# Kernel tuning notes

Hardware: AMD Instinct MI355X
Metric: run time of the kernel (lower is better)

## Reference

```python
import jax, jax.numpy as jnp
import numpy as np

D = 1024
H = 16
DH = D // H  # 64
EPS = 1e-6


def setup_inputs() -> dict:
    key = jax.random.key(0)
    ks = jax.random.split(key, 8)
    N, NQ, NK = 8, 1024, 1024
    queries = jax.random.normal(ks[0], (N, NQ, D), dtype=jnp.float32)
    keys = jax.random.normal(ks[1], (N, NK, D), dtype=jnp.float32)
    values = jax.random.normal(ks[2], (N, NK, D), dtype=jnp.float32)
    mask = jax.random.uniform(ks[3], (H * N, NQ, NK), dtype=jnp.float32)
    s = 1.0 / np.sqrt(D)
    Wq = jax.random.normal(ks[4], (H, DH, D), dtype=jnp.float32) * s  # per-head Linear(d, d_head) weights
    Wk = jax.random.normal(ks[5], (H, DH, D), dtype=jnp.float32) * s
    Wv = jax.random.normal(ks[6], (H, DH, D), dtype=jnp.float32) * s
    Wo = jax.random.normal(ks[7], (D, D), dtype=jnp.float32) * s
    return {"queries": queries, "keys": keys, "values": values, "mask": mask,
            "Wq": Wq, "Wk": Wk, "Wv": Wv, "Wo": Wo}


def reference(queries, keys, values, mask, Wq, Wk, Wv, Wo):
    N, NQ, _ = queries.shape
    NK = keys.shape[1]
    # per-head projections, fused into one batched einsum (head-major like torch.cat(dim=0))
    q = jnp.einsum('nqd,hed->hnqe', queries, Wq)  # [H, N, NQ, DH]
    k = jnp.einsum('nkd,hed->hnke', keys, Wk)
    v = jnp.einsum('nkd,hed->hnke', values, Wv)
    scores = jnp.einsum('hnqe,hnke->hnqk', q, k) / jnp.sqrt(jnp.float32(DH))
    att = jax.nn.softmax(scores, axis=-1)  # [H, N, NQ, NK]
    m = mask.reshape(H, N, NQ, NK)
    att = att * m
    att = att / (att.sum(axis=-1, keepdims=True) + EPS)
    o = jnp.einsum('hnqk,hnke->hnqe', att, v)  # [H, N, NQ, DH]
    # concat heads along feature dim: [N, NQ, H*DH]
    o = o.transpose(1, 2, 0, 3).reshape(N, NQ, D)
    return o @ Wo.T
```

## Files before the change

### kernel.cpp

```cpp
#include <hip/hip_runtime.h>
#include <stdint.h>

#define DEV static __device__ __forceinline__

typedef __attribute__((ext_vector_type(8))) short shortx8;
typedef __attribute__((ext_vector_type(4))) float floatx4;
typedef __attribute__((ext_vector_type(4))) unsigned short ushortx4;
typedef __attribute__((ext_vector_type(4))) unsigned int uintx4;


DEV unsigned short f2bf(float x) {
  unsigned int u = __float_as_uint(x);
  u += 0x7fffu + ((u >> 16) & 1u);
  return (unsigned short)(u >> 16);
}

DEV unsigned int cvtpk(float lo, float hi) {
  unsigned int r;
  asm("v_cvt_pk_bf16_f32 %0, %1, %2" : "=v"(r) : "v"(lo), "v"(hi));
  return r;
}

DEV void async16(const void* g, void* l) {
  __builtin_amdgcn_global_load_lds(
      (const __attribute__((address_space(1))) void*)g,
      (__attribute__((address_space(3))) void*)l, 16, 0, 0);
}

__global__ __launch_bounds__(256) void cast_all(
    const float* __restrict__ xq, const float* __restrict__ xk, const float* __restrict__ xv,
    const float* __restrict__ wq, const float* __restrict__ wk, const float* __restrict__ wv,
    const float* __restrict__ wo,
    unsigned short* __restrict__ oxq, unsigned short* __restrict__ oxk, unsigned short* __restrict__ oxv,
    unsigned short* __restrict__ owq, unsigned short* __restrict__ owk, unsigned short* __restrict__ owv,
    unsigned short* __restrict__ owo) {
  int b = blockIdx.x;
  const float* in;
  unsigned short* out;
  size_t i;
  if (b < 12288) {
    int which = b >> 12;
    in = which == 0 ? xq : (which == 1 ? xk : xv);
    out = which == 0 ? oxq : (which == 1 ? oxk : oxv);
    i = (size_t)(b & 4095) * 256 + threadIdx.x;
  } else {
    int bb = b - 12288;
    int which = bb >> 9;
    in = which == 0 ? wq : (which == 1 ? wk : (which == 2 ? wv : wo));
    out = which == 0 ? owq : (which == 1 ? owk : (which == 2 ? owv : owo));
    i = (size_t)(bb & 511) * 256 + threadIdx.x;
  }
  const floatx4* src = (const floatx4*)in;
  floatx4 a = src[2 * i];
  floatx4 c = src[2 * i + 1];
  uintx4 o;
  o[0] = cvtpk(a[0], a[1]);
  o[1] = cvtpk(a[2], a[3]);
  o[2] = cvtpk(c[0], c[1]);
  o[3] = cvtpk(c[2], c[3]);
  ((uintx4*)out)[i] = o;
}


__global__ __launch_bounds__(256) void gemm_qkv(
    const unsigned short* __restrict__ Xq, const unsigned short* __restrict__ Xk,
    const unsigned short* __restrict__ Xv,
    const unsigned short* __restrict__ Bq, const unsigned short* __restrict__ Bk,
    const unsigned short* __restrict__ Bv,
    unsigned short* __restrict__ Oq, unsigned short* __restrict__ Ok,
    unsigned short* __restrict__ Ov) {
  __shared__ __align__(16) unsigned short As[128 * 32];
  __shared__ __align__(16) unsigned short Bs[128 * 32];
  const int z = blockIdx.z;
  const unsigned short* A = z == 0 ? Xq : (z == 1 ? Xk : Xv);
  const unsigned short* B = z == 0 ? Bq : (z == 1 ? Bk : Bv);
  unsigned short* O = z == 0 ? Oq : (z == 1 ? Ok : Ov);

  const int tid  = threadIdx.x;
  const int lane = tid & 63;
  const int wave = tid >> 6;
  const int wm = wave & 1, wn = wave >> 1;
  const int l16 = lane & 15, quad = lane >> 4;
  const int rowBase = blockIdx.y * 128;
  const int colBase = blockIdx.x * 128;

  floatx4 acc[4][4] = {};

  for (int kt = 0; kt < 32; ++kt) {
    __syncthreads();
#pragma unroll
    for (int i = 0; i < 2; ++i) {
      int c = i * 256 + tid;
      int r = c >> 2, kq = c & 3;
      async16(A + (size_t)(rowBase + r) * 1024 + kt * 32 + kq * 8, &As[c * 8]);
      async16(B + (size_t)(colBase + r) * 1024 + kt * 32 + kq * 8, &Bs[c * 8]);
    }
    __syncthreads();
    shortx8 af[4], bfr[4];
#pragma unroll
    for (int t = 0; t < 4; ++t) {
      af[t]  = *(const shortx8*)&As[(wm * 64 + t * 16 + l16) * 32 + quad * 8];
      bfr[t] = *(const shortx8*)&Bs[(wn * 64 + t * 16 + l16) * 32 + quad * 8];
    }
#pragma unroll
    for (int mt = 0; mt < 4; ++mt)
#pragma unroll
      for (int nt = 0; nt < 4; ++nt)
        acc[mt][nt] = __builtin_amdgcn_mfma_f32_16x16x32_bf16(af[mt], bfr[nt], acc[mt][nt], 0, 0, 0);
  }

#pragma unroll
  for (int mt = 0; mt < 4; ++mt) {
#pragma unroll
    for (int nt = 0; nt < 4; ++nt) {
      int col  = colBase + wn * 64 + nt * 16 + l16;
      int row0 = rowBase + wm * 64 + mt * 16 + quad * 4;
      int h = col >> 6, e = col & 63;
      if (z != 2) {
#pragma unroll
        for (int r = 0; r < 4; ++r) {
          int row = row0 + r;
          int n = row >> 10, seq = row & 1023;
          O[(size_t)((h * 8 + n) * 1024 + seq) * 64 + e] = f2bf(acc[mt][nt][r]);
        }
      } else {
        int n = row0 >> 10, seq0 = row0 & 1023;
        ushortx4 pk;
        pk[0] = f2bf(acc[mt][nt][0]); pk[1] = f2bf(acc[mt][nt][1]);
        pk[2] = f2bf(acc[mt][nt][2]); pk[3] = f2bf(acc[mt][nt][3]);
        *(ushortx4*)&O[(size_t)((h * 8 + n) * 64 + e) * 1024 + seq0] = pk;
      }
    }
  }
}

__global__ __launch_bounds__(256) void gemm_out(const unsigned short* __restrict__ A,
                                                const unsigned short* __restrict__ B,
                                                float* __restrict__ O) {
  __shared__ __align__(16) unsigned short As[128 * 32];
  __shared__ __align__(16) unsigned short Bs[128 * 32];
  const int tid  = threadIdx.x;
  const int lane = tid & 63;
  const int wave = tid >> 6;
  const int wm = wave & 1, wn = wave >> 1;
  const int l16 = lane & 15, quad = lane >> 4;
  const int rowBase = blockIdx.y * 128;
  const int colBase = blockIdx.x * 128;

  floatx4 acc[4][4] = {};

  for (int kt = 0; kt < 32; ++kt) {
    __syncthreads();
#pragma unroll
    for (int i = 0; i < 2; ++i) {
      int c = i * 256 + tid;
      int r = c >> 2, kq = c & 3;
      async16(A + (size_t)(rowBase + r) * 1024 + kt * 32 + kq * 8, &As[c * 8]);
      async16(B + (size_t)(colBase + r) * 1024 + kt * 32 + kq * 8, &Bs[c * 8]);
    }
    __syncthreads();
    shortx8 af[4], bfr[4];
#pragma unroll
    for (int t = 0; t < 4; ++t) {
      af[t]  = *(const shortx8*)&As[(wm * 64 + t * 16 + l16) * 32 + quad * 8];
      bfr[t] = *(const shortx8*)&Bs[(wn * 64 + t * 16 + l16) * 32 + quad * 8];
    }
#pragma unroll
    for (int mt = 0; mt < 4; ++mt)
#pragma unroll
      for (int nt = 0; nt < 4; ++nt)
        acc[mt][nt] = __builtin_amdgcn_mfma_f32_16x16x32_bf16(af[mt], bfr[nt], acc[mt][nt], 0, 0, 0);
  }

#pragma unroll
  for (int mt = 0; mt < 4; ++mt)
#pragma unroll
    for (int nt = 0; nt < 4; ++nt) {
      int col  = colBase + wn * 64 + nt * 16 + l16;
      int row0 = rowBase + wm * 64 + mt * 16 + quad * 4;
#pragma unroll
      for (int r = 0; r < 4; ++r)
        O[(size_t)(row0 + r) * 1024 + col] = acc[mt][nt][r];
    }
}

__global__ __launch_bounds__(256) void attn_kernel(const unsigned short* __restrict__ Q,
                                                   const unsigned short* __restrict__ K,
                                                   const unsigned short* __restrict__ Vt,
                                                   const float* __restrict__ mask,
                                                   unsigned short* __restrict__ O) {
  __shared__ __align__(16) unsigned short Ks[2][64 * 64];
  __shared__ __align__(16) unsigned short Vs[2][64 * 64];
  __shared__ __align__(16) unsigned short Pl[4 * 32 * 72];
  const int tid = threadIdx.x, lane = tid & 63, wave = tid >> 6;
  const int l16 = lane & 15, quad = lane >> 4;
  const int d = blockIdx.y * 8 + blockIdx.x;
  const int hn = (d & 7) * 16 + ((d >> 3) & 15);
  const int qt = d >> 7;
  const int h = hn >> 3, n = hn & 7;
  const float SC = 0.18033688011112042f;
  const int swz = (l16 & 7) << 4;

  const unsigned short* Qb = Q + (size_t)hn * 65536;
  const unsigned short* Kb = K + (size_t)hn * 65536;
  const unsigned short* Vb = Vt + (size_t)hn * 65536;
  const float* Mb = mask + (size_t)hn * 1048576;
  const int q0 = qt * 128 + wave * 32;

  auto stage = [&](int buf, int kbase) {
#pragma unroll
    for (int i = 0; i < 2; ++i) {
      int c = i * 256 + tid;
      int r = c >> 3;
      int lo = ((c & 7) * 16) ^ ((r & 7) << 4);
      async16((const char*)Kb + (size_t)(kbase + r) * 128 + lo,
              (char*)&Ks[buf][0] + c * 16);
      async16((const char*)Vb + (size_t)r * 2048 + (size_t)kbase * 2 + lo,
              (char*)&Vs[buf][0] + c * 16);
    }
  };

  stage(0, 0);

  shortx8 qf[2][2];
#pragma unroll
  for (int rt = 0; rt < 2; ++rt)
#pragma unroll
    for (int ks = 0; ks < 2; ++ks)
      qf[rt][ks] = *(const shortx8*)&Qb[(size_t)(q0 + rt * 16 + l16) * 64 + ks * 32 + quad * 8];

  floatx4 oacc[2][4] = {};
  float lsum[2][4] = {};
  unsigned short* Pw = &Pl[wave * 32 * 72];

  __syncthreads();

  for (int kt = 0; kt < 16; ++kt) {
    const int kbase = kt * 64;
    const int buf = kt & 1;

    if (kt < 15) stage(buf ^ 1, kbase + 64);

    shortx8 kf[4][2];
#pragma unroll
    for (int ct = 0; ct < 4; ++ct)
#pragma unroll
      for (int ks = 0; ks < 2; ++ks) {
        int R = ct * 16 + l16;
        kf[ct][ks] = *(const shortx8*)((const char*)&Ks[buf][0] + R * 128 +
                                       ((ks * 64 + quad * 16) ^ swz));
      }

#pragma unroll
    for (int rt = 0; rt < 2; ++rt) {
      float mk[4][4];
      const float* Mrow = Mb + (size_t)(q0 + rt * 16 + quad * 4) * 1024 + kbase;
#pragma unroll
      for (int r = 0; r < 4; ++r)
#pragma unroll
        for (int ct = 0; ct < 4; ++ct)
          mk[ct][r] = Mrow[(size_t)r * 1024 + ct * 16 + l16];

      floatx4 s[4] = {};
      __builtin_amdgcn_s_setprio(1);
#pragma unroll
      for (int ct = 0; ct < 4; ++ct)
#pragma unroll
        for (int ks = 0; ks < 2; ++ks)
          s[ct] = __builtin_amdgcn_mfma_f32_16x16x32_bf16(qf[rt][ks], kf[ct][ks], s[ct], 0, 0, 0);
      __builtin_amdgcn_s_setprio(0);

#pragma unroll
      for (int ct = 0; ct < 4; ++ct) {
        float pm[4];
#pragma unroll
        for (int r = 0; r < 4; ++r) {
          float p = exp2f(s[ct][r] * SC);
          pm[r] = p * mk[ct][r];
          lsum[rt][r] += pm[r];
        }
        unsigned int d01 = cvtpk(pm[0], pm[1]);
        unsigned int d23 = cvtpk(pm[2], pm[3]);
        int base = (rt * 16 + quad * 4) * 72 + ct * 16 + l16;
        Pw[base]       = (unsigned short)d01;
        Pw[base + 72]  = (unsigned short)(d01 >> 16);
        Pw[base + 144] = (unsigned short)d23;
        Pw[base + 216] = (unsigned short)(d23 >> 16);
      }
    }

    shortx8 pf[2][2];
#pragma unroll
    for (int rt = 0; rt < 2; ++rt)
#pragma unroll
      for (int ks = 0; ks < 2; ++ks)
        pf[rt][ks] = *(const shortx8*)&Pw[(rt * 16 + l16) * 72 + ks * 32 + quad * 8];
#pragma unroll
    for (int nt = 0; nt < 4; ++nt) {
      int R = nt * 16 + l16;
      shortx8 vf0 = *(const shortx8*)((const char*)&Vs[buf][0] + R * 128 + ((quad * 16) ^ swz));
      shortx8 vf1 = *(const shortx8*)((const char*)&Vs[buf][0] + R * 128 + ((64 + quad * 16) ^ swz));
      __builtin_amdgcn_s_setprio(1);
#pragma unroll
      for (int rt = 0; rt < 2; ++rt) {
        oacc[rt][nt] = __builtin_amdgcn_mfma_f32_16x16x32_bf16(pf[rt][0], vf0, oacc[rt][nt], 0, 0, 0);
        oacc[rt][nt] = __builtin_amdgcn_mfma_f32_16x16x32_bf16(pf[rt][1], vf1, oacc[rt][nt], 0, 0, 0);
      }
      __builtin_amdgcn_s_setprio(0);
    }

    __syncthreads();
  }

#pragma unroll
  for (int off = 8; off >= 1; off >>= 1)
#pragma unroll
    for (int rt = 0; rt < 2; ++rt)
#pragma unroll
      for (int r = 0; r < 4; ++r)
        lsum[rt][r] += __shfl_xor(lsum[rt][r], off, 64);

  float inv[2][4];
#pragma unroll
  for (int rt = 0; rt < 2; ++rt)
#pragma unroll
    for (int r = 0; r < 4; ++r)
      inv[rt][r] = 1.0f / (lsum[rt][r] + 1e-20f);

#pragma unroll
  for (int rt = 0; rt < 2; ++rt)
#pragma unroll
    for (int nt = 0; nt < 4; ++nt)
#pragma unroll
      for (int r = 0; r < 4; ++r) {
        int qg = q0 + rt * 16 + quad * 4 + r;
        O[(size_t)(n * 1024 + qg) * 1024 + h * 64 + nt * 16 + l16] =
            f2bf(oacc[rt][nt][r] * inv[rt][r]);
      }
}

extern "C" void kernel_launch(void* const* d_in, const int* in_sizes, int n_in,
                              void* d_out, int out_size, void* d_ws, size_t ws_size,
                              hipStream_t stream) {
  const float* queries = (const float*)d_in[0];
  const float* keys    = (const float*)d_in[1];
  const float* values  = (const float*)d_in[2];
  const float* mask    = (const float*)d_in[3];
  const float* Wq      = (const float*)d_in[4];
  const float* Wk      = (const float*)d_in[5];
  const float* Wv      = (const float*)d_in[6];
  const float* Wo      = (const float*)d_in[7];

  char* ws = (char*)d_ws;
  unsigned short* Xq  = (unsigned short*)(ws);
  unsigned short* Xk  = (unsigned short*)(ws + (16u << 20));
  unsigned short* Xv  = (unsigned short*)(ws + (32u << 20));
  unsigned short* Wqb = (unsigned short*)(ws + (48u << 20));
  unsigned short* Wkb = (unsigned short*)(ws + (50u << 20));
  unsigned short* Wvb = (unsigned short*)(ws + (52u << 20));
  unsigned short* Wob = (unsigned short*)(ws + (54u << 20));
  unsigned short* Qp  = (unsigned short*)(ws + (56u << 20));
  unsigned short* Kp  = (unsigned short*)(ws + (72u << 20));
  unsigned short* Vt  = (unsigned short*)(ws + (88u << 20));
  unsigned short* Ob  = Xq;
  float* out = (float*)d_out;

  dim3 blk(256);

  cast_all<<<dim3(14336), blk, 0, stream>>>(queries, keys, values, Wq, Wk, Wv, Wo,
                                            Xq, Xk, Xv, Wqb, Wkb, Wvb, Wob);
  gemm_qkv<<<dim3(8, 64, 3), blk, 0, stream>>>(Xq, Xk, Xv, Wqb, Wkb, Wvb, Qp, Kp, Vt);
  attn_kernel<<<dim3(8, 128), blk, 0, stream>>>(Qp, Kp, Vt, mask, Ob);
  gemm_out<<<dim3(8, 64), blk, 0, stream>>>(Ob, Wob, out);
}
```

Baseline: 923.8 us.

## Deepen GEMM K-tile with swizzled LDS and double attention query rows per wave

```diff
diff --git a/kernel.cpp b/kernel.cpp
--- a/kernel.cpp
+++ b/kernel.cpp
@@ -62,6 +62,49 @@
 }
 
 
+DEV void gemm_core(const unsigned short* __restrict__ A,
+                   const unsigned short* __restrict__ B,
+                   unsigned short* As, unsigned short* Bs,
+                   floatx4 (&acc)[4][4],
+                   int rowBase, int colBase, int tid) {
+  const int lane = tid & 63;
+  const int wave = tid >> 6;
+  const int wm = wave & 1, wn = wave >> 1;
+  const int l16 = lane & 15, quad = lane >> 4;
+  const int swz = (l16 & 7) << 4;
+
+  for (int kt = 0; kt < 16; ++kt) {
+    __syncthreads();
+#pragma unroll
+    for (int i = 0; i < 4; ++i) {
+      int c = i * 256 + tid;
+      int r = c >> 3;
+      int lo = ((c & 7) * 16) ^ ((r & 7) << 4);
+      async16((const char*)A + (size_t)(rowBase + r) * 2048 + kt * 128 + lo,
+              (char*)As + c * 16);
+      async16((const char*)B + (size_t)(colBase + r) * 2048 + kt * 128 + lo,
+              (char*)Bs + c * 16);
+    }
+    __syncthreads();
+#pragma unroll
+    for (int ks = 0; ks < 2; ++ks) {
+      shortx8 af[4], bfr[4];
+#pragma unroll
+      for (int t = 0; t < 4; ++t) {
+        int Ra = wm * 64 + t * 16 + l16;
+        int Rb = wn * 64 + t * 16 + l16;
+        af[t]  = *(const shortx8*)((const char*)As + Ra * 128 + ((ks * 64 + quad * 16) ^ swz));
+        bfr[t] = *(const shortx8*)((const char*)Bs + Rb * 128 + ((ks * 64 + quad * 16) ^ swz));
+      }
+#pragma unroll
+      for (int mt = 0; mt < 4; ++mt)
+#pragma unroll
+        for (int nt = 0; nt < 4; ++nt)
+          acc[mt][nt] = __builtin_amdgcn_mfma_f32_16x16x32_bf16(af[mt], bfr[nt], acc[mt][nt], 0, 0, 0);
+    }
+  }
+}
+
 __global__ __launch_bounds__(256) void gemm_qkv(
     const unsigned short* __restrict__ Xq, const unsigned short* __restrict__ Xk,
     const unsigned short* __restrict__ Xv,
@@ -69,8 +112,8 @@
     const unsigned short* __restrict__ Bv,
     unsigned short* __restrict__ Oq, unsigned short* __restrict__ Ok,
     unsigned short* __restrict__ Ov) {
-  __shared__ __align__(16) unsigned short As[128 * 32];
-  __shared__ __align__(16) unsigned short Bs[128 * 32];
+  __shared__ __align__(16) unsigned short As[128 * 64];
+  __shared__ __align__(16) unsigned short Bs[128 * 64];
   const int z = blockIdx.z;
   const unsigned short* A = z == 0 ? Xq : (z == 1 ? Xk : Xv);
   const unsigned short* B = z == 0 ? Bq : (z == 1 ? Bk : Bv);
@@ -85,29 +128,7 @@
   const int colBase = blockIdx.x * 128;
 
   floatx4 acc[4][4] = {};
-
-  for (int kt = 0; kt < 32; ++kt) {
-    __syncthreads();
-#pragma unroll
-    for (int i = 0; i < 2; ++i) {
-      int c = i * 256 + tid;
-      int r = c >> 2, kq = c & 3;
-      async16(A + (size_t)(rowBase + r) * 1024 + kt * 32 + kq * 8, &As[c * 8]);
-      async16(B + (size_t)(colBase + r) * 1024 + kt * 32 + kq * 8, &Bs[c * 8]);
-    }
-    __syncthreads();
-    shortx8 af[4], bfr[4];
-#pragma unroll
-    for (int t = 0; t < 4; ++t) {
-      af[t]  = *(const shortx8*)&As[(wm * 64 + t * 16 + l16) * 32 + quad * 8];
-      bfr[t] = *(const shortx8*)&Bs[(wn * 64 + t * 16 + l16) * 32 + quad * 8];
-    }
-#pragma unroll
-    for (int mt = 0; mt < 4; ++mt)
-#pragma unroll
-      for (int nt = 0; nt < 4; ++nt)
-        acc[mt][nt] = __builtin_amdgcn_mfma_f32_16x16x32_bf16(af[mt], bfr[nt], acc[mt][nt], 0, 0, 0);
-  }
+  gemm_core(A, B, As, Bs, acc, rowBase, colBase, tid);
 
 #pragma unroll
   for (int mt = 0; mt < 4; ++mt) {
@@ -137,8 +158,8 @@
 __global__ __launch_bounds__(256) void gemm_out(const unsigned short* __restrict__ A,
                                                 const unsigned short* __restrict__ B,
                                                 float* __restrict__ O) {
-  __shared__ __align__(16) unsigned short As[128 * 32];
-  __shared__ __align__(16) unsigned short Bs[128 * 32];
+  __shared__ __align__(16) unsigned short As[128 * 64];
+  __shared__ __align__(16) unsigned short Bs[128 * 64];
   const int tid  = threadIdx.x;
   const int lane = tid & 63;
   const int wave = tid >> 6;
@@ -148,29 +169,7 @@
   const int colBase = blockIdx.x * 128;
 
   floatx4 acc[4][4] = {};
-
-  for (int kt = 0; kt < 32; ++kt) {
-    __syncthreads();
-#pragma unroll
-    for (int i = 0; i < 2; ++i) {
-      int c = i * 256 + tid;
-      int r = c >> 2, kq = c & 3;
-      async16(A + (size_t)(rowBase + r) * 1024 + kt * 32 + kq * 8, &As[c * 8]);
-      async16(B + (size_t)(colBase + r) * 1024 + kt * 32 + kq * 8, &Bs[c * 8]);
-    }
-    __syncthreads();
-    shortx8 af[4], bfr[4];
-#pragma unroll
-    for (int t = 0; t < 4; ++t) {
-      af[t]  = *(const shortx8*)&As[(wm * 64 + t * 16 + l16) * 32 + quad * 8];
-      bfr[t] = *(const shortx8*)&Bs[(wn * 64 + t * 16 + l16) * 32 + quad * 8];
-    }
-#pragma unroll
-    for (int mt = 0; mt < 4; ++mt)
-#pragma unroll
-      for (int nt = 0; nt < 4; ++nt)
-        acc[mt][nt] = __builtin_amdgcn_mfma_f32_16x16x32_bf16(af[mt], bfr[nt], acc[mt][nt], 0, 0, 0);
-  }
+  gemm_core(A, B, As, Bs, acc, rowBase, colBase, tid);
 
 #pragma unroll
   for (int mt = 0; mt < 4; ++mt)
@@ -184,11 +183,11 @@
     }
 }
 
-__global__ __launch_bounds__(256) void attn_kernel(const unsigned short* __restrict__ Q,
-                                                   const unsigned short* __restrict__ K,
-                                                   const unsigned short* __restrict__ Vt,
-                                                   const float* __restrict__ mask,
-                                                   unsigned short* __restrict__ O) {
+__global__ __launch_bounds__(256, 2) void attn_kernel(const unsigned short* __restrict__ Q,
+                                                      const unsigned short* __restrict__ K,
+                                                      const unsigned short* __restrict__ Vt,
+                                                      const float* __restrict__ mask,
+                                                      unsigned short* __restrict__ O) {
   __shared__ __align__(16) unsigned short Ks[2][64 * 64];
   __shared__ __align__(16) unsigned short Vs[2][64 * 64];
   __shared__ __align__(16) unsigned short Pl[4 * 32 * 72];
@@ -205,7 +204,7 @@
   const unsigned short* Kb = K + (size_t)hn * 65536;
   const unsigned short* Vb = Vt + (size_t)hn * 65536;
   const float* Mb = mask + (size_t)hn * 1048576;
-  const int q0 = qt * 128 + wave * 32;
+  const int q0 = qt * 256 + wave * 64;
 
   auto stage = [&](int buf, int kbase) {
 #pragma unroll
@@ -222,15 +221,15 @@
 
   stage(0, 0);
 
-  shortx8 qf[2][2];
-#pragma unroll
-  for (int rt = 0; rt < 2; ++rt)
+  shortx8 qf[4][2];
+#pragma unroll
+  for (int s = 0; s < 4; ++s)
 #pragma unroll
     for (int ks = 0; ks < 2; ++ks)
-      qf[rt][ks] = *(const shortx8*)&Qb[(size_t)(q0 + rt * 16 + l16) * 64 + ks * 32 + quad * 8];
-
-  floatx4 oacc[2][4] = {};
-  float lsum[2][4] = {};
+      qf[s][ks] = *(const shortx8*)&Qb[(size_t)(q0 + s * 16 + l16) * 64 + ks * 32 + quad * 8];
+
+  floatx4 oacc[4][4] = {};
+  float lsum[4][4] = {};
   unsigned short* Pw = &Pl[wave * 32 * 72];
 
   __syncthreads();
@@ -241,71 +240,76 @@
 
     if (kt < 15) stage(buf ^ 1, kbase + 64);
 
-    shortx8 kf[4][2];
-#pragma unroll
-    for (int ct = 0; ct < 4; ++ct)
+    shortx8 kf[4][2], vf[4][2];
+#pragma unroll
+    for (int ct = 0; ct < 4; ++ct) {
+      int R = ct * 16 + l16;
 #pragma unroll
       for (int ks = 0; ks < 2; ++ks) {
-        int R = ct * 16 + l16;
         kf[ct][ks] = *(const shortx8*)((const char*)&Ks[buf][0] + R * 128 +
                                        ((ks * 64 + quad * 16) ^ swz));
-      }
-
-#pragma unroll
-    for (int rt = 0; rt < 2; ++rt) {
-      float mk[4][4];
-      const float* Mrow = Mb + (size_t)(q0 + rt * 16 + quad * 4) * 1024 + kbase;
-#pragma unroll
-      for (int r = 0; r < 4; ++r)
+        vf[ct][ks] = *(const shortx8*)((const char*)&Vs[buf][0] + R * 128 +
+                                       ((ks * 64 + quad * 16) ^ swz));
+      }
+    }
+
+#pragma unroll
+    for (int pass = 0; pass < 2; ++pass) {
+#pragma unroll
+      for (int rtL = 0; rtL < 2; ++rtL) {
+        const int s = pass * 2 + rtL;
+        float mk[4][4];
+        const float* Mrow = Mb + (size_t)(q0 + s * 16 + quad * 4) * 1024 + kbase;
+#pragma unroll
+        for (int r = 0; r < 4; ++r)
+#pragma unroll
+          for (int ct = 0; ct < 4; ++ct)
+            mk[ct][r] = Mrow[(size_t)r * 1024 + ct * 16 + l16];
+
+        floatx4 sc[4] = {};
+        __builtin_amdgcn_s_setprio(1);
 #pragma unroll
         for (int ct = 0; ct < 4; ++ct)
-          mk[ct][r] = Mrow[(size_t)r * 1024 + ct * 16 + l16];
-
-      floatx4 s[4] = {};
+#pragma unroll
+          for (int ks = 0; ks < 2; ++ks)
+            sc[ct] = __builtin_amdgcn_mfma_f32_16x16x32_bf16(qf[s][ks], kf[ct][ks], sc[ct], 0, 0, 0);
+        __builtin_amdgcn_s_setprio(0);
+
+#pragma unroll
+        for (int ct = 0; ct < 4; ++ct) {
+          float pm[4];
+#pragma unroll
+          for (int r = 0; r < 4; ++r) {
+            float p = exp2f(sc[ct][r] * SC);
+            pm[r] = p * mk[ct][r];
+            lsum[s][r] += pm[r];
+          }
+          unsigned int d01 = cvtpk(pm[0], pm[1]);
+          unsigned int d23 = cvtpk(pm[2], pm[3]);
+          int base = (rtL * 16 + quad * 4) * 72 + ct * 16 + l16;
+          Pw[base]       = (unsigned short)d01;
+          Pw[base + 72]  = (unsigned short)(d01 >> 16);
+          Pw[base + 144] = (unsigned short)d23;
+          Pw[base + 216] = (unsigned short)(d23 >> 16);
+        }
+      }
+
+      shortx8 pf[2][2];
+#pragma unroll
+      for (int rtL = 0; rtL < 2; ++rtL)
+#pragma unroll
+        for (int ks = 0; ks < 2; ++ks)
+          pf[rtL][ks] = *(const shortx8*)&Pw[(rtL * 16 + l16) * 72 + ks * 32 + quad * 8];
       __builtin_amdgcn_s_setprio(1);
 #pragma unroll
-      for (int ct = 0; ct < 4; ++ct)
-#pragma unroll
-        for (int ks = 0; ks < 2; ++ks)
-          s[ct] = __builtin_amdgcn_mfma_f32_16x16x32_bf16(qf[rt][ks], kf[ct][ks], s[ct], 0, 0, 0);
-      __builtin_amdgcn_s_setprio(0);
-
-#pragma unroll
-      for (int ct = 0; ct < 4; ++ct) {
-        float pm[4];
-#pragma unroll
-        for (int r = 0; r < 4; ++r) {
-          float p = exp2f(s[ct][r] * SC);
-          pm[r] = p * mk[ct][r];
-          lsum[rt][r] += pm[r];
+      for (int nt = 0; nt < 4; ++nt)
+#pragma unroll
+        for (int rtL = 0; rtL < 2; ++rtL) {
+          oacc[pass * 2 + rtL][nt] = __builtin_amdgcn_mfma_f32_16x16x32_bf16(
+              pf[rtL][0], vf[nt][0], oacc[pass * 2 + rtL][nt], 0, 0, 0);
+          oacc[pass * 2 + rtL][nt] = __builtin_amdgcn_mfma_f32_16x16x32_bf16(
+              pf[rtL][1], vf[nt][1], oacc[pass * 2 + rtL][nt], 0, 0, 0);
         }
-        unsigned int d01 = cvtpk(pm[0], pm[1]);
-        unsigned int d23 = cvtpk(pm[2], pm[3]);
-        int base = (rt * 16 + quad * 4) * 72 + ct * 16 + l16;
-        Pw[base]       = (unsigned short)d01;
-        Pw[base + 72]  = (unsigned short)(d01 >> 16);
-        Pw[base + 144] = (unsigned short)d23;
-        Pw[base + 216] = (unsigned short)(d23 >> 16);
-      }
-    }
-
-    shortx8 pf[2][2];
-#pragma unroll
-    for (int rt = 0; rt < 2; ++rt)
-#pragma unroll
-      for (int ks = 0; ks < 2; ++ks)
-        pf[rt][ks] = *(const shortx8*)&Pw[(rt * 16 + l16) * 72 + ks * 32 + quad * 8];
-#pragma unroll
-    for (int nt = 0; nt < 4; ++nt) {
-      int R = nt * 16 + l16;
-      shortx8 vf0 = *(const shortx8*)((const char*)&Vs[buf][0] + R * 128 + ((quad * 16) ^ swz));
-      shortx8 vf1 = *(const shortx8*)((const char*)&Vs[buf][0] + R * 128 + ((64 + quad * 16) ^ swz));
-      __builtin_amdgcn_s_setprio(1);
-#pragma unroll
-      for (int rt = 0; rt < 2; ++rt) {
-        oacc[rt][nt] = __builtin_amdgcn_mfma_f32_16x16x32_bf16(pf[rt][0], vf0, oacc[rt][nt], 0, 0, 0);
-        oacc[rt][nt] = __builtin_amdgcn_mfma_f32_16x16x32_bf16(pf[rt][1], vf1, oacc[rt][nt], 0, 0, 0);
-      }
       __builtin_amdgcn_s_setprio(0);
     }
 
@@ -315,27 +319,27 @@
 #pragma unroll
   for (int off = 8; off >= 1; off >>= 1)
 #pragma unroll
-    for (int rt = 0; rt < 2; ++rt)
+    for (int s = 0; s < 4; ++s)
 #pragma unroll
       for (int r = 0; r < 4; ++r)
-        lsum[rt][r] += __shfl_xor(lsum[rt][r], off, 64);
-
-  float inv[2][4];
-#pragma unroll
-  for (int rt = 0; rt < 2; ++rt)
+        lsum[s][r] += __shfl_xor(lsum[s][r], off, 64);
+
+  float inv[4][4];
+#pragma unroll
+  for (int s = 0; s < 4; ++s)
 #pragma unroll
     for (int r = 0; r < 4; ++r)
-      inv[rt][r] = 1.0f / (lsum[rt][r] + 1e-20f);
-
-#pragma unroll
-  for (int rt = 0; rt < 2; ++rt)
+      inv[s][r] = 1.0f / (lsum[s][r] + 1e-20f);
+
+#pragma unroll
+  for (int s = 0; s < 4; ++s)
 #pragma unroll
     for (int nt = 0; nt < 4; ++nt)
 #pragma unroll
       for (int r = 0; r < 4; ++r) {
-        int qg = q0 + rt * 16 + quad * 4 + r;
+        int qg = q0 + s * 16 + quad * 4 + r;
         O[(size_t)(n * 1024 + qg) * 1024 + h * 64 + nt * 16 + l16] =
-            f2bf(oacc[rt][nt][r] * inv[rt][r]);
+            f2bf(oacc[s][nt][r] * inv[s][r]);
       }
 }
 
@@ -370,6 +374,6 @@
   cast_all<<<dim3(14336), blk, 0, stream>>>(queries, keys, values, Wq, Wk, Wv, Wo,
                                             Xq, Xk, Xv, Wqb, Wkb, Wvb, Wob);
   gemm_qkv<<<dim3(8, 64, 3), blk, 0, stream>>>(Xq, Xk, Xv, Wqb, Wkb, Wvb, Qp, Kp, Vt);
-  attn_kernel<<<dim3(8, 128), blk, 0, stream>>>(Qp, Kp, Vt, mask, Ob);
+  attn_kernel<<<dim3(8, 64), blk, 0, stream>>>(Qp, Kp, Vt, mask, Ob);
   gemm_out<<<dim3(8, 64), blk, 0, stream>>>(Ob, Wob, out);
 }
```

Result: no change. 908.8 us (-1.6%).
